# Kernel tuning notes

Measured on AMD Instinct MI355X. Metric: run time of the kernel, lower is better.

Reference implementation:

```python
import jax, jax.numpy as jnp
import numpy as np

# Module scale: T timesteps, N nodes, E directed edges
T, N, E = 6, 20000, 320000
IN_F, HID, OUT_F, K = 11, 64, 3, 2  # K=2 Chebyshev graph conv


def setup_inputs() -> dict:
    key = jax.random.key(0)
    ks = jax.random.split(key, 8)
    X_seq = jax.random.normal(ks[0], (T, N, IN_F), dtype=jnp.float32)
    # col 6 is physical time; make it a monotone ramp so dt != 0 between steps
    X_seq = X_seq.at[:, :, 6].set(jnp.arange(T, dtype=jnp.float32)[:, None] * 0.01)
    edge = jax.random.randint(ks[1], (2, E), 0, N)
    s = 0.05
    # 6 ChebConvs inside GConvGRU, stacked by gate order (z, r, h)
    Wx = jax.random.normal(ks[2], (3, K, IN_F, HID), dtype=jnp.float32) * s
    Wh = jax.random.normal(ks[3], (3, K, HID, HID), dtype=jnp.float32) * s
    bx = jax.random.normal(ks[4], (3, HID), dtype=jnp.float32) * s
    bh = jax.random.normal(ks[5], (3, HID), dtype=jnp.float32) * s
    head_W = jax.random.normal(ks[6], (HID, OUT_F), dtype=jnp.float32) * s
    head_b = jnp.zeros((OUT_F,), dtype=jnp.float32)
    return dict(X_seq=X_seq, edge=edge, Wx=Wx, bx=bx, Wh=Wh, bh=bh,
                head_W=head_W, head_b=head_b)


def _cheb(x, W, b, src, dst, ew, n):
    # PyG ChebConv (sym norm, lambda_max=2): Lhat = -D^-1/2 A D^-1/2
    # K=2: out = T0(x) @ W0 + T1(x) @ W1 + b, T0 = x, T1 = Lhat x
    out = x @ W[0]
    Tx1 = jax.ops.segment_sum(ew[:, None] * x[src], dst, num_segments=n)  # [N, F]
    return out + Tx1 @ W[1] + b


def _forward(X_seq, edge, Wx, bx, Wh, bh, head_W, head_b):
    n = X_seq.shape[1]
    src, dst = edge[0], edge[1]
    deg = jax.ops.segment_sum(jnp.ones((edge.shape[1],), X_seq.dtype), src,
                              num_segments=n)
    dis = jnp.where(deg > 0, jax.lax.rsqrt(jnp.maximum(deg, 1.0)), 0.0)
    ew = -dis[src] * dis[dst]  # scaled Laplacian edge weights

    def cell(x, h):  # GConvGRU cell
        Z = jax.nn.sigmoid(_cheb(x, Wx[0], bx[0], src, dst, ew, n)
                           + _cheb(h, Wh[0], bh[0], src, dst, ew, n))
        R = jax.nn.sigmoid(_cheb(x, Wx[1], bx[1], src, dst, ew, n)
                           + _cheb(h, Wh[1], bh[1], src, dst, ew, n))
        Ht = jnp.tanh(_cheb(x, Wx[2], bx[2], src, dst, ew, n)
                      + _cheb(h * R, Wh[2], bh[2], src, dst, ew, n))
        return Z * h + (1.0 - Z) * Ht

    X_prev = jnp.concatenate([X_seq[:1], X_seq[:-1]], axis=0)

    def step(carry, xs):
        h, u_prev = carry  # u_prev is detached (stop_gradient) like u.detach()
        x_t, x_pm1, t = xs
        dt = x_t[:, 6] - x_pm1[:, 6]
        dt = jnp.where(t == 0, jnp.ones_like(dt), dt)  # guard; t=0 branch discarded
        v = (u_prev - x_pm1[:, 3:6]) / dt[:, None]
        x_mod = x_t.at[:, 3:6].set(u_prev).at[:, 8:11].set(v)
        x_in = jnp.where(t == 0, x_t, x_mod)
        h = cell(x_in, h)
        u = h @ head_W + head_b
        return (h, jax.lax.stop_gradient(u)), u

    h0 = jnp.zeros((n, Wh.shape[-1]), X_seq.dtype)
    u0 = jnp.zeros((n, head_W.shape[-1]), X_seq.dtype)
    ts = jnp.arange(X_seq.shape[0])
    _, outs = jax.lax.scan(step, (h0, u0), (X_seq, X_prev, ts))
    return outs  # [T, N, out_f]


def reference(X_seq, edge, Wx, bx, Wh, bh, head_W, head_b):
    return _forward(X_seq, edge, Wx, bx, Wh, bh, head_W, head_b)
```

## Files before the change

kernel.cpp:

```cpp
#include <hip/hip_runtime.h>
#include <hip/hip_fp16.h>
#include <math.h>

#define TSTEPS 6
#define NN 20000
#define NE 320000
#define INF 11
#define XPAD 16
#define HID 64
#define OUTF 3
#define NPW 4

__device__ __forceinline__ float bcast(float v, int l) {
    return __uint_as_float(__builtin_amdgcn_readlane(__float_as_uint(v), l));
}

__device__ __forceinline__ float tanh_safe(float a) {
    float e2 = __expf(-2.0f * fabsf(a));
    float t = (1.0f - e2) / (1.0f + e2);
    return copysignf(t, a);
}


__global__ void k_deg(const int* __restrict__ src, float* __restrict__ deg, int E) {
    int e = blockIdx.x * blockDim.x + threadIdx.x;
    if (e < E) atomicAdd(&deg[src[e]], 1.0f);
}

__global__ void k_dis(float* deg, int n) {
    int i = blockIdx.x * blockDim.x + threadIdx.x;
    if (i < n) {
        float d = deg[i];
        deg[i] = d > 0.0f ? rsqrtf(fmaxf(d, 1.0f)) : 0.0f;
    }
}

__global__ void k_ew(const int* __restrict__ src, const int* __restrict__ dst,
                     const float* __restrict__ dis, float* __restrict__ ew, int E) {
    int e = blockIdx.x * blockDim.x + threadIdx.x;
    if (e < E) ew[e] = -dis[src[e]] * dis[dst[e]];
}

__global__ void k_indeg(const int* __restrict__ dst, int* __restrict__ indeg, int E) {
    int e = blockIdx.x * blockDim.x + threadIdx.x;
    if (e < E) atomicAdd(&indeg[dst[e]], 1);
}

__global__ __launch_bounds__(1024) void k_scan(const int* __restrict__ in,
                                               int* __restrict__ out, int n) {
    __shared__ int buf[1024];
    __shared__ int carry;
    if (threadIdx.x == 0) carry = 0;
    __syncthreads();
    for (int base = 0; base < n; base += 1024) {
        int i = base + (int)threadIdx.x;
        int v = (i < n) ? in[i] : 0;
        buf[threadIdx.x] = v;
        __syncthreads();
        for (int off = 1; off < 1024; off <<= 1) {
            int t = (threadIdx.x >= (unsigned)off) ? buf[threadIdx.x - off] : 0;
            __syncthreads();
            buf[threadIdx.x] += t;
            __syncthreads();
        }
        if (i < n) out[i] = carry + buf[threadIdx.x] - v;
        __syncthreads();
        if (threadIdx.x == 0) carry += buf[1023];
        __syncthreads();
    }
    if (threadIdx.x == 0) out[n] = carry;
}

__global__ void k_fill(const int* __restrict__ src, const int* __restrict__ dst,
                       const float* __restrict__ ew, int* __restrict__ cursor,
                       int2* __restrict__ pack, int E) {
    int e = blockIdx.x * blockDim.x + threadIdx.x;
    if (e >= E) return;
    int pos = atomicAdd(&cursor[dst[e]], 1);
    int2 v;
    v.x = src[e];
    v.y = __float_as_int(ew[e]);
    pack[pos] = v;
}

__global__ void k_packh4(const float* __restrict__ Wh, float4* __restrict__ out) {
    int idx = blockIdx.x * blockDim.x + threadIdx.x;
    if (idx >= HID * HID) return;
    int j = idx >> 6, f = idx & 63;
    float4 v;
    v.x = Wh[((0 * 2 + 0) * HID + j) * HID + f];
    v.y = Wh[((0 * 2 + 1) * HID + j) * HID + f];
    v.z = Wh[((1 * 2 + 0) * HID + j) * HID + f];
    v.w = Wh[((1 * 2 + 1) * HID + j) * HID + f];
    out[idx] = v;
}
__global__ void k_packh2(const float* __restrict__ Wh, float2* __restrict__ out) {
    int idx = blockIdx.x * blockDim.x + threadIdx.x;
    if (idx >= HID * HID) return;
    int j = idx >> 6, f = idx & 63;
    float2 v;
    v.x = Wh[((2 * 2 + 0) * HID + j) * HID + f];
    v.y = Wh[((2 * 2 + 1) * HID + j) * HID + f];
    out[idx] = v;
}
__global__ void k_packx4(const float* __restrict__ Wx, float4* __restrict__ out) {
    int idx = blockIdx.x * blockDim.x + threadIdx.x;
    if (idx >= INF * HID) return;
    int i = idx >> 6, f = idx & 63;
    float4 v;
    v.x = Wx[((0 * 2 + 0) * INF + i) * HID + f];
    v.y = Wx[((0 * 2 + 1) * INF + i) * HID + f];
    v.z = Wx[((1 * 2 + 0) * INF + i) * HID + f];
    v.w = Wx[((1 * 2 + 1) * INF + i) * HID + f];
    out[idx] = v;
}
__global__ void k_packx2(const float* __restrict__ Wx, float2* __restrict__ out) {
    int idx = blockIdx.x * blockDim.x + threadIdx.x;
    if (idx >= INF * HID) return;
    int i = idx >> 6, f = idx & 63;
    float2 v;
    v.x = Wx[((2 * 2 + 0) * INF + i) * HID + f];
    v.y = Wx[((2 * 2 + 1) * INF + i) * HID + f];
    out[idx] = v;
}


__global__ void k_xin0(const float* __restrict__ Xt, float* __restrict__ xin,
                       __half* __restrict__ xin16, int n) {
    int i = blockIdx.x * blockDim.x + threadIdx.x;
    if (i >= n) return;
    const float* xt = Xt + (size_t)i * INF;
    float* xo = xin + (size_t)i * XPAD;
    __half* xh = xin16 + (size_t)i * XPAD;
#pragma unroll
    for (int k = 0; k < INF; ++k) { float v = xt[k]; xo[k] = v; xh[k] = __float2half(v); }
#pragma unroll
    for (int k = INF; k < XPAD; ++k) { xo[k] = 0.0f; xh[k] = __float2half(0.0f); }
}

__global__ void k_xin(const float* __restrict__ Xt, const float* __restrict__ Xp,
                      const float* __restrict__ uprev, float* __restrict__ xin,
                      __half* __restrict__ xin16, int n) {
    int i = blockIdx.x * blockDim.x + threadIdx.x;
    if (i >= n) return;
    const float* xt = Xt + (size_t)i * INF;
    const float* xp = Xp + (size_t)i * INF;
    const float* up = uprev + (size_t)i * OUTF;
    float* xo = xin + (size_t)i * XPAD;
    __half* xh = xin16 + (size_t)i * XPAD;
    float dt = xt[6] - xp[6];
    float inv = 1.0f / dt;
    float v[XPAD];
    v[0] = xt[0]; v[1] = xt[1]; v[2] = xt[2];
    v[3] = up[0]; v[4] = up[1]; v[5] = up[2];
    v[6] = xt[6]; v[7] = xt[7];
    v[8] = (up[0] - xp[3]) * inv;
    v[9] = (up[1] - xp[4]) * inv;
    v[10] = (up[2] - xp[5]) * inv;
    v[11] = 0.0f; v[12] = 0.0f; v[13] = 0.0f; v[14] = 0.0f; v[15] = 0.0f;
#pragma unroll
    for (int k = 0; k < XPAD; ++k) { xo[k] = v[k]; xh[k] = __float2half(v[k]); }
}

__global__ __launch_bounds__(256) void k_gz(
    const int* __restrict__ rowstart, const int2* __restrict__ pack,
    const float* __restrict__ xin, const __half* __restrict__ xin16,
    const __half* __restrict__ h16,
    const float4* __restrict__ Wx4, const float* __restrict__ bx,
    const float4* __restrict__ Wh4, const float* __restrict__ bh,
    float* __restrict__ t1x, __half* __restrict__ Zb16,
    __half* __restrict__ hr16, int n) {
    int wid = __builtin_amdgcn_readfirstlane(
        (int)((blockIdx.x * blockDim.x + threadIdx.x) >> 6));
    int wbase = wid * NPW;
    int lane = threadIdx.x & 63;
    int f16i = lane & 15;
    if (wbase >= n) return;

    float thg[NPW], axv[NPW], hv[NPW];
#pragma unroll
    for (int nn = 0; nn < NPW; ++nn) {
        int node = wbase + nn;
        int s = rowstart[node], e = rowstart[node + 1];
        float a0 = 0, a1 = 0, a2 = 0, a3 = 0;
        float c0 = 0, c1 = 0, c2 = 0, c3 = 0;
        int p = s;
        for (; p + 3 < e; p += 4) {
            int2 e0 = pack[p], e1 = pack[p + 1], e2 = pack[p + 2], e3 = pack[p + 3];
            float w0 = __int_as_float(e0.y), w1 = __int_as_float(e1.y);
            float w2 = __int_as_float(e2.y), w3 = __int_as_float(e3.y);
            a0 = fmaf(w0, __half2float(h16[(size_t)e0.x * HID + lane]), a0);
            a1 = fmaf(w1, __half2float(h16[(size_t)e1.x * HID + lane]), a1);
            a2 = fmaf(w2, __half2float(h16[(size_t)e2.x * HID + lane]), a2);
            a3 = fmaf(w3, __half2float(h16[(size_t)e3.x * HID + lane]), a3);
            c0 = fmaf(w0, __half2float(xin16[(size_t)e0.x * XPAD + f16i]), c0);
            c1 = fmaf(w1, __half2float(xin16[(size_t)e1.x * XPAD + f16i]), c1);
            c2 = fmaf(w2, __half2float(xin16[(size_t)e2.x * XPAD + f16i]), c2);
            c3 = fmaf(w3, __half2float(xin16[(size_t)e3.x * XPAD + f16i]), c3);
        }
        for (; p < e; ++p) {
            int2 e0 = pack[p];
            float w0 = __int_as_float(e0.y);
            a0 = fmaf(w0, __half2float(h16[(size_t)e0.x * HID + lane]), a0);
            c0 = fmaf(w0, __half2float(xin16[(size_t)e0.x * XPAD + f16i]), c0);
        }
        thg[nn] = (a0 + a1) + (a2 + a3);
        axv[nn] = (c0 + c1) + (c2 + c3);
        hv[nn] = __half2float(h16[(size_t)node * HID + lane]);
    }
#pragma unroll
    for (int nn = 0; nn < NPW; ++nn)
        if (lane < 16) t1x[(size_t)(wbase + nn) * XPAD + lane] = axv[nn];

    float xrow = xin[(size_t)wbase * XPAD + lane];
    float b0z = bx[0 * HID + lane] + bh[0 * HID + lane];
    float b0r = bx[1 * HID + lane] + bh[1 * HID + lane];
    float az[NPW], ar[NPW];
#pragma unroll
    for (int nn = 0; nn < NPW; ++nn) { az[nn] = b0z; ar[nn] = b0r; }
#pragma unroll
    for (int i = 0; i < INF; ++i) {
        float4 w = Wx4[i * HID + lane];
#pragma unroll
        for (int nn = 0; nn < NPW; ++nn) {
            float xv = bcast(xrow, nn * XPAD + i);
            float tv = bcast(axv[nn], i);
            az[nn] = fmaf(xv, w.x, fmaf(tv, w.y, az[nn]));
            ar[nn] = fmaf(xv, w.z, fmaf(tv, w.w, ar[nn]));
        }
    }
#pragma unroll 8
    for (int j = 0; j < HID; ++j) {
        float4 w = Wh4[j * HID + lane];
#pragma unroll
        for (int nn = 0; nn < NPW; ++nn) {
            float hj = bcast(hv[nn], j);
            float tj = bcast(thg[nn], j);
            az[nn] = fmaf(hj, w.x, fmaf(tj, w.y, az[nn]));
            ar[nn] = fmaf(hj, w.z, fmaf(tj, w.w, ar[nn]));
        }
    }
#pragma unroll
    for (int nn = 0; nn < NPW; ++nn) {
        int node = wbase + nn;
        float Z = 1.0f / (1.0f + __expf(-az[nn]));
        float R = 1.0f / (1.0f + __expf(-ar[nn]));
        Zb16[(size_t)node * HID + lane] = __float2half(Z);
        hr16[(size_t)node * HID + lane] = __float2half(hv[nn] * R);
    }
}

__global__ __launch_bounds__(256) void k_gc(
    const int* __restrict__ rowstart, const int2* __restrict__ pack,
    const float* __restrict__ xin, const float* __restrict__ t1x,
    float* __restrict__ h, __half* __restrict__ h16,
    const __half* __restrict__ hr16,
    const float2* __restrict__ Wx2, const float* __restrict__ bx,
    const float2* __restrict__ Wh2, const float* __restrict__ bh,
    const __half* __restrict__ Zb16,
    const float* __restrict__ hw, const float* __restrict__ hb,
    float* __restrict__ out, int n) {
    int wid = __builtin_amdgcn_readfirstlane(
        (int)((blockIdx.x * blockDim.x + threadIdx.x) >> 6));
    int wbase = wid * NPW;
    int lane = threadIdx.x & 63;
    if (wbase >= n) return;

    float thg[NPW], hrv[NPW];
#pragma unroll
    for (int nn = 0; nn < NPW; ++nn) {
        int node = wbase + nn;
        int s = rowstart[node], e = rowstart[node + 1];
        float a0 = 0, a1 = 0, a2 = 0, a3 = 0;
        int p = s;
        for (; p + 3 < e; p += 4) {
            int2 e0 = pack[p], e1 = pack[p + 1], e2 = pack[p + 2], e3 = pack[p + 3];
            a0 = fmaf(__int_as_float(e0.y), __half2float(hr16[(size_t)e0.x * HID + lane]), a0);
            a1 = fmaf(__int_as_float(e1.y), __half2float(hr16[(size_t)e1.x * HID + lane]), a1);
            a2 = fmaf(__int_as_float(e2.y), __half2float(hr16[(size_t)e2.x * HID + lane]), a2);
            a3 = fmaf(__int_as_float(e3.y), __half2float(hr16[(size_t)e3.x * HID + lane]), a3);
        }
        for (; p < e; ++p) {
            int2 e0 = pack[p];
            a0 = fmaf(__int_as_float(e0.y), __half2float(hr16[(size_t)e0.x * HID + lane]), a0);
        }
        thg[nn] = (a0 + a1) + (a2 + a3);
        hrv[nn] = __half2float(hr16[(size_t)node * HID + lane]);
    }

    float xrow = xin[(size_t)wbase * XPAD + lane];
    float trow = t1x[(size_t)wbase * XPAD + lane];
    float b0 = bx[2 * HID + lane] + bh[2 * HID + lane];
    float ah[NPW];
#pragma unroll
    for (int nn = 0; nn < NPW; ++nn) ah[nn] = b0;
#pragma unroll
    for (int i = 0; i < INF; ++i) {
        float2 w = Wx2[i * HID + lane];
#pragma unroll
        for (int nn = 0; nn < NPW; ++nn) {
            float xv = bcast(xrow, nn * XPAD + i);
            float tv = bcast(trow, nn * XPAD + i);
            ah[nn] = fmaf(xv, w.x, fmaf(tv, w.y, ah[nn]));
        }
    }
#pragma unroll 8
    for (int j = 0; j < HID; ++j) {
        float2 w = Wh2[j * HID + lane];
#pragma unroll
        for (int nn = 0; nn < NPW; ++nn) {
            float hj = bcast(hrv[nn], j);
            float tj = bcast(thg[nn], j);
            ah[nn] = fmaf(hj, w.x, fmaf(tj, w.y, ah[nn]));
        }
    }
#pragma unroll
    for (int nn = 0; nn < NPW; ++nn) {
        int node = wbase + nn;
        float Ht = tanh_safe(ah[nn]);
        float z = __half2float(Zb16[(size_t)node * HID + lane]);
        float hv = h[(size_t)node * HID + lane];
        float hnew = z * hv + (1.0f - z) * Ht;
        h[(size_t)node * HID + lane] = hnew;
        h16[(size_t)node * HID + lane] = __float2half(hnew);
#pragma unroll
        for (int o = 0; o < OUTF; ++o) {
            float v = hnew * hw[lane * OUTF + o];
            for (int off = 32; off; off >>= 1) v += __shfl_down(v, off);
            if (lane == 0) out[(size_t)node * OUTF + o] = v + hb[o];
        }
    }
}

extern "C" void kernel_launch(void* const* d_in, const int* in_sizes, int n_in,
                              void* d_out, int out_size, void* d_ws, size_t ws_size,
                              hipStream_t stream) {
    const float* X_seq = (const float*)d_in[0];
    const int* edge = (const int*)d_in[1];
    const float* Wx = (const float*)d_in[2];
    const float* bx = (const float*)d_in[3];
    const float* Wh = (const float*)d_in[4];
    const float* bh = (const float*)d_in[5];
    const float* head_W = (const float*)d_in[6];
    const float* head_b = (const float*)d_in[7];
    float* out = (float*)d_out;

    const int* src = edge;
    const int* dst = edge + NE;

    float* ws = (float*)d_ws;
    float4* Wh4g = (float4*)ws;
    float4* Wx4g = (float4*)(ws + 16384);
    float2* Wh2c = (float2*)(ws + 16384 + 2816);
    float2* Wx2c = (float2*)(ws + 16384 + 2816 + 8192);
    float* fbase = ws + 28800;
    float* dis   = fbase;
    float* ew    = dis + NN;
    float* xin   = ew + NE;
    float* t1x   = xin + NN * XPAD;
    float* h     = t1x + NN * XPAD;
    int* indeg    = (int*)(h + NN * HID);
    int* rowstart = indeg + NN;
    int* cursor   = rowstart + NN + 2;
    int2* pack    = (int2*)(cursor + NN);
    __half* h16   = (__half*)(pack + NE);
    __half* hr16  = h16 + (size_t)NN * HID;
    __half* Zb16  = hr16 + (size_t)NN * HID;
    __half* xin16 = Zb16 + (size_t)NN * HID;

    hipMemsetAsync(dis, 0, NN * sizeof(float), stream);
    hipMemsetAsync(indeg, 0, NN * sizeof(int), stream);
    k_deg<<<(NE + 255) / 256, 256, 0, stream>>>(src, dis, NE);
    k_dis<<<(NN + 255) / 256, 256, 0, stream>>>(dis, NN);
    k_ew<<<(NE + 255) / 256, 256, 0, stream>>>(src, dst, dis, ew, NE);
    k_indeg<<<(NE + 255) / 256, 256, 0, stream>>>(dst, indeg, NE);
    k_scan<<<1, 1024, 0, stream>>>(indeg, rowstart, NN);
    hipMemcpyAsync(cursor, rowstart, NN * sizeof(int), hipMemcpyDeviceToDevice, stream);
    k_fill<<<(NE + 255) / 256, 256, 0, stream>>>(src, dst, ew, cursor, pack, NE);
    k_packh4<<<(HID * HID + 255) / 256, 256, 0, stream>>>(Wh, Wh4g);
    k_packh2<<<(HID * HID + 255) / 256, 256, 0, stream>>>(Wh, Wh2c);
    k_packx4<<<(INF * HID + 255) / 256, 256, 0, stream>>>(Wx, Wx4g);
    k_packx2<<<(INF * HID + 255) / 256, 256, 0, stream>>>(Wx, Wx2c);

    hipMemsetAsync(h, 0, NN * HID * sizeof(float), stream);
    hipMemsetAsync(h16, 0, NN * HID * sizeof(__half), stream);

    const int fused_grid = (NN + 4 * NPW - 1) / (4 * NPW);

    for (int t = 0; t < TSTEPS; ++t) {
        const float* Xt = X_seq + (size_t)t * NN * INF;

        if (t == 0) {
            k_xin0<<<(NN + 255) / 256, 256, 0, stream>>>(Xt, xin, xin16, NN);
        } else {
            const float* Xp = X_seq + (size_t)(t - 1) * NN * INF;
            const float* uprev = out + (size_t)(t - 1) * NN * OUTF;
            k_xin<<<(NN + 255) / 256, 256, 0, stream>>>(Xt, Xp, uprev, xin, xin16, NN);
        }

        k_gz<<<fused_grid, 256, 0, stream>>>(rowstart, pack, xin, xin16, h16,
                                             Wx4g, bx, Wh4g, bh,
                                             t1x, Zb16, hr16, NN);

        k_gc<<<fused_grid, 256, 0, stream>>>(rowstart, pack, xin, t1x, h, h16, hr16,
                                             Wx2c, bx, Wh2c, bh, Zb16,
                                             head_W, head_b,
                                             out + (size_t)t * NN * OUTF, NN);
    }
}
```

Baseline: 531.3 us.

## Pad CSR rows to multiples of 8, fuse input prep into gate kernel, parallelize setup

Each CSR row is padded to a multiple of 8 zero-weight entries, so the gather loops run an 8-wide unrolled body with no scalar tail. In k_gz the x-feature aggregation is split across four 16-lane groups and combined with shuffles. The per-step k_xin kernel is removed: the next step's input row is built inside k_gc from the freshly computed head outputs. Setup is also consolidated: one counting kernel, a three-phase parallel scan replacing the single-block scan, edge weights computed inside fill, one weight-pack kernel, and a zeroing kernel. The padding adds extra zero-weight gathers from node 0, and the pack buffer must be memset each call.

```diff
diff --git a/kernel.cpp b/kernel.cpp
--- a/kernel.cpp
+++ b/kernel.cpp
@@ -10,6 +10,8 @@
 #define HID 64
 #define OUTF 3
 #define NPW 4
+#define EPMAX (NE + 7 * NN)
+#define NB ((NN + 255) / 256)
 
 __device__ __forceinline__ float bcast(float v, int l) {
     return __uint_as_float(__builtin_amdgcn_readlane(__float_as_uint(v), l));
@@ -22,108 +24,124 @@
 }
 
 
-__global__ void k_deg(const int* __restrict__ src, float* __restrict__ deg, int E) {
+__global__ void k_cnt(const int* __restrict__ src, const int* __restrict__ dst,
+                      int* __restrict__ degi, int* __restrict__ indeg, int E) {
     int e = blockIdx.x * blockDim.x + threadIdx.x;
-    if (e < E) atomicAdd(&deg[src[e]], 1.0f);
-}
-
-__global__ void k_dis(float* deg, int n) {
+    if (e >= E) return;
+    atomicAdd(&degi[src[e]], 1);
+    atomicAdd(&indeg[dst[e]], 1);
+}
+
+__global__ void k_dis(const int* __restrict__ degi, float* __restrict__ dis, int n) {
     int i = blockIdx.x * blockDim.x + threadIdx.x;
     if (i < n) {
-        float d = deg[i];
-        deg[i] = d > 0.0f ? rsqrtf(fmaxf(d, 1.0f)) : 0.0f;
-    }
-}
-
-__global__ void k_ew(const int* __restrict__ src, const int* __restrict__ dst,
-                     const float* __restrict__ dis, float* __restrict__ ew, int E) {
-    int e = blockIdx.x * blockDim.x + threadIdx.x;
-    if (e < E) ew[e] = -dis[src[e]] * dis[dst[e]];
-}
-
-__global__ void k_indeg(const int* __restrict__ dst, int* __restrict__ indeg, int E) {
-    int e = blockIdx.x * blockDim.x + threadIdx.x;
-    if (e < E) atomicAdd(&indeg[dst[e]], 1);
-}
-
-__global__ __launch_bounds__(1024) void k_scan(const int* __restrict__ in,
-                                               int* __restrict__ out, int n) {
-    __shared__ int buf[1024];
-    __shared__ int carry;
-    if (threadIdx.x == 0) carry = 0;
+        float d = (float)degi[i];
+        dis[i] = d > 0.0f ? rsqrtf(fmaxf(d, 1.0f)) : 0.0f;
+    }
+}
+
+__global__ __launch_bounds__(256) void k_scanA(const int* __restrict__ indeg,
+                                               int* __restrict__ part,
+                                               int* __restrict__ bsum, int n) {
+    int idx = blockIdx.x * 256 + threadIdx.x;
+    int lane = threadIdx.x & 63, wv = threadIdx.x >> 6;
+    int v = (idx < n) ? ((indeg[idx] + 7) & ~7) : 0;
+#pragma unroll
+    for (int off = 1; off < 64; off <<= 1) {
+        int t = __shfl_up(v, off);
+        if (lane >= off) v += t;
+    }
+    __shared__ int wsum[4];
+    if (lane == 63) wsum[wv] = v;
     __syncthreads();
-    for (int base = 0; base < n; base += 1024) {
-        int i = base + (int)threadIdx.x;
-        int v = (i < n) ? in[i] : 0;
-        buf[threadIdx.x] = v;
-        __syncthreads();
-        for (int off = 1; off < 1024; off <<= 1) {
-            int t = (threadIdx.x >= (unsigned)off) ? buf[threadIdx.x - off] : 0;
-            __syncthreads();
-            buf[threadIdx.x] += t;
-            __syncthreads();
-        }
-        if (i < n) out[i] = carry + buf[threadIdx.x] - v;
-        __syncthreads();
-        if (threadIdx.x == 0) carry += buf[1023];
-        __syncthreads();
-    }
-    if (threadIdx.x == 0) out[n] = carry;
+    int add = 0;
+    for (int w = 0; w < wv; ++w) add += wsum[w];
+    v += add;
+    if (idx < n) part[idx] = v;
+    if (threadIdx.x == 255) bsum[blockIdx.x] = v;
+}
+
+__global__ __launch_bounds__(128) void k_scanB(const int* __restrict__ bsum,
+                                               int* __restrict__ boff, int nb) {
+    int tid = threadIdx.x;
+    int lane = tid & 63, wv = tid >> 6;
+    int orig = (tid < nb) ? bsum[tid] : 0;
+    int v = orig;
+#pragma unroll
+    for (int off = 1; off < 64; off <<= 1) {
+        int t = __shfl_up(v, off);
+        if (lane >= off) v += t;
+    }
+    __shared__ int w0;
+    if (lane == 63 && wv == 0) w0 = v;
+    __syncthreads();
+    if (wv == 1) v += w0;
+    if (tid < nb) boff[tid] = v - orig;
+}
+
+__global__ __launch_bounds__(256) void k_scanC(const int* __restrict__ indeg,
+                                               int* __restrict__ part,
+                                               const int* __restrict__ boff,
+                                               int* __restrict__ cursor, int n) {
+    int idx = blockIdx.x * 256 + threadIdx.x;
+    if (idx >= n) return;
+    int pd = (indeg[idx] + 7) & ~7;
+    int incl = part[idx] + boff[blockIdx.x];
+    int excl = incl - pd;
+    part[idx] = excl;
+    cursor[idx] = excl;
+    if (idx == n - 1) part[n] = incl;
 }
 
 __global__ void k_fill(const int* __restrict__ src, const int* __restrict__ dst,
-                       const float* __restrict__ ew, int* __restrict__ cursor,
+                       const float* __restrict__ dis, int* __restrict__ cursor,
                        int2* __restrict__ pack, int E) {
     int e = blockIdx.x * blockDim.x + threadIdx.x;
     if (e >= E) return;
-    int pos = atomicAdd(&cursor[dst[e]], 1);
+    int s = src[e], d = dst[e];
+    int pos = atomicAdd(&cursor[d], 1);
     int2 v;
-    v.x = src[e];
-    v.y = __float_as_int(ew[e]);
+    v.x = s;
+    v.y = __float_as_int(-dis[s] * dis[d]);
     pack[pos] = v;
 }
 
-__global__ void k_packh4(const float* __restrict__ Wh, float4* __restrict__ out) {
+__global__ void k_pack(const float* __restrict__ Wh, const float* __restrict__ Wx,
+                       float4* __restrict__ Wh4, float2* __restrict__ Wh2,
+                       float4* __restrict__ Wx4, float2* __restrict__ Wx2) {
     int idx = blockIdx.x * blockDim.x + threadIdx.x;
-    if (idx >= HID * HID) return;
-    int j = idx >> 6, f = idx & 63;
-    float4 v;
-    v.x = Wh[((0 * 2 + 0) * HID + j) * HID + f];
-    v.y = Wh[((0 * 2 + 1) * HID + j) * HID + f];
-    v.z = Wh[((1 * 2 + 0) * HID + j) * HID + f];
-    v.w = Wh[((1 * 2 + 1) * HID + j) * HID + f];
-    out[idx] = v;
-}
-__global__ void k_packh2(const float* __restrict__ Wh, float2* __restrict__ out) {
-    int idx = blockIdx.x * blockDim.x + threadIdx.x;
-    if (idx >= HID * HID) return;
-    int j = idx >> 6, f = idx & 63;
-    float2 v;
-    v.x = Wh[((2 * 2 + 0) * HID + j) * HID + f];
-    v.y = Wh[((2 * 2 + 1) * HID + j) * HID + f];
-    out[idx] = v;
-}
-__global__ void k_packx4(const float* __restrict__ Wx, float4* __restrict__ out) {
-    int idx = blockIdx.x * blockDim.x + threadIdx.x;
-    if (idx >= INF * HID) return;
-    int i = idx >> 6, f = idx & 63;
-    float4 v;
-    v.x = Wx[((0 * 2 + 0) * INF + i) * HID + f];
-    v.y = Wx[((0 * 2 + 1) * INF + i) * HID + f];
-    v.z = Wx[((1 * 2 + 0) * INF + i) * HID + f];
-    v.w = Wx[((1 * 2 + 1) * INF + i) * HID + f];
-    out[idx] = v;
-}
-__global__ void k_packx2(const float* __restrict__ Wx, float2* __restrict__ out) {
-    int idx = blockIdx.x * blockDim.x + threadIdx.x;
-    if (idx >= INF * HID) return;
-    int i = idx >> 6, f = idx & 63;
-    float2 v;
-    v.x = Wx[((2 * 2 + 0) * INF + i) * HID + f];
-    v.y = Wx[((2 * 2 + 1) * INF + i) * HID + f];
-    out[idx] = v;
-}
-
+    if (idx < HID * HID) {
+        int j = idx >> 6, f = idx & 63;
+        float4 v4;
+        v4.x = Wh[((0 * 2 + 0) * HID + j) * HID + f];
+        v4.y = Wh[((0 * 2 + 1) * HID + j) * HID + f];
+        v4.z = Wh[((1 * 2 + 0) * HID + j) * HID + f];
+        v4.w = Wh[((1 * 2 + 1) * HID + j) * HID + f];
+        Wh4[idx] = v4;
+        float2 v2;
+        v2.x = Wh[((2 * 2 + 0) * HID + j) * HID + f];
+        v2.y = Wh[((2 * 2 + 1) * HID + j) * HID + f];
+        Wh2[idx] = v2;
+    } else if (idx < HID * HID + INF * HID) {
+        int k = idx - HID * HID;
+        int i = k >> 6, f = k & 63;
+        float4 v4;
+        v4.x = Wx[((0 * 2 + 0) * INF + i) * HID + f];
+        v4.y = Wx[((0 * 2 + 1) * INF + i) * HID + f];
+        v4.z = Wx[((1 * 2 + 0) * INF + i) * HID + f];
+        v4.w = Wx[((1 * 2 + 1) * INF + i) * HID + f];
+        Wx4[k] = v4;
+        float2 v2;
+        v2.x = Wx[((2 * 2 + 0) * INF + i) * HID + f];
+        v2.y = Wx[((2 * 2 + 1) * INF + i) * HID + f];
+        Wx2[k] = v2;
+    }
+}
+
+__global__ void k_hzero(float* __restrict__ h, __half* __restrict__ h16, int nel) {
+    int i = blockIdx.x * blockDim.x + threadIdx.x;
+    if (i < nel) { h[i] = 0.0f; h16[i] = __float2half(0.0f); }
+}
 
 __global__ void k_xin0(const float* __restrict__ Xt, float* __restrict__ xin,
                        __half* __restrict__ xin16, int n) {
@@ -138,29 +156,6 @@
     for (int k = INF; k < XPAD; ++k) { xo[k] = 0.0f; xh[k] = __float2half(0.0f); }
 }
 
-__global__ void k_xin(const float* __restrict__ Xt, const float* __restrict__ Xp,
-                      const float* __restrict__ uprev, float* __restrict__ xin,
-                      __half* __restrict__ xin16, int n) {
-    int i = blockIdx.x * blockDim.x + threadIdx.x;
-    if (i >= n) return;
-    const float* xt = Xt + (size_t)i * INF;
-    const float* xp = Xp + (size_t)i * INF;
-    const float* up = uprev + (size_t)i * OUTF;
-    float* xo = xin + (size_t)i * XPAD;
-    __half* xh = xin16 + (size_t)i * XPAD;
-    float dt = xt[6] - xp[6];
-    float inv = 1.0f / dt;
-    float v[XPAD];
-    v[0] = xt[0]; v[1] = xt[1]; v[2] = xt[2];
-    v[3] = up[0]; v[4] = up[1]; v[5] = up[2];
-    v[6] = xt[6]; v[7] = xt[7];
-    v[8] = (up[0] - xp[3]) * inv;
-    v[9] = (up[1] - xp[4]) * inv;
-    v[10] = (up[2] - xp[5]) * inv;
-    v[11] = 0.0f; v[12] = 0.0f; v[13] = 0.0f; v[14] = 0.0f; v[15] = 0.0f;
-#pragma unroll
-    for (int k = 0; k < XPAD; ++k) { xo[k] = v[k]; xh[k] = __float2half(v[k]); }
-}
 
 __global__ __launch_bounds__(256) void k_gz(
     const int* __restrict__ rowstart, const int2* __restrict__ pack,
@@ -174,7 +169,7 @@
         (int)((blockIdx.x * blockDim.x + threadIdx.x) >> 6));
     int wbase = wid * NPW;
     int lane = threadIdx.x & 63;
-    int f16i = lane & 15;
+    int f16i = lane & 15, eo = lane >> 4;
     if (wbase >= n) return;
 
     float thg[NPW], axv[NPW], hv[NPW];
@@ -183,29 +178,34 @@
         int node = wbase + nn;
         int s = rowstart[node], e = rowstart[node + 1];
         float a0 = 0, a1 = 0, a2 = 0, a3 = 0;
-        float c0 = 0, c1 = 0, c2 = 0, c3 = 0;
-        int p = s;
-        for (; p + 3 < e; p += 4) {
-            int2 e0 = pack[p], e1 = pack[p + 1], e2 = pack[p + 2], e3 = pack[p + 3];
+        float c0 = 0, c1 = 0;
+        for (int p = s; p < e; p += 8) {
+            int2 e0 = pack[p],     e1 = pack[p + 1], e2 = pack[p + 2], e3 = pack[p + 3];
+            int2 e4 = pack[p + 4], e5 = pack[p + 5], e6 = pack[p + 6], e7 = pack[p + 7];
             float w0 = __int_as_float(e0.y), w1 = __int_as_float(e1.y);
             float w2 = __int_as_float(e2.y), w3 = __int_as_float(e3.y);
+            float w4 = __int_as_float(e4.y), w5 = __int_as_float(e5.y);
+            float w6 = __int_as_float(e6.y), w7 = __int_as_float(e7.y);
             a0 = fmaf(w0, __half2float(h16[(size_t)e0.x * HID + lane]), a0);
             a1 = fmaf(w1, __half2float(h16[(size_t)e1.x * HID + lane]), a1);
             a2 = fmaf(w2, __half2float(h16[(size_t)e2.x * HID + lane]), a2);
             a3 = fmaf(w3, __half2float(h16[(size_t)e3.x * HID + lane]), a3);
-            c0 = fmaf(w0, __half2float(xin16[(size_t)e0.x * XPAD + f16i]), c0);
-            c1 = fmaf(w1, __half2float(xin16[(size_t)e1.x * XPAD + f16i]), c1);
-            c2 = fmaf(w2, __half2float(xin16[(size_t)e2.x * XPAD + f16i]), c2);
-            c3 = fmaf(w3, __half2float(xin16[(size_t)e3.x * XPAD + f16i]), c3);
-        }
-        for (; p < e; ++p) {
-            int2 e0 = pack[p];
-            float w0 = __int_as_float(e0.y);
-            a0 = fmaf(w0, __half2float(h16[(size_t)e0.x * HID + lane]), a0);
-            c0 = fmaf(w0, __half2float(xin16[(size_t)e0.x * XPAD + f16i]), c0);
+            a0 = fmaf(w4, __half2float(h16[(size_t)e4.x * HID + lane]), a0);
+            a1 = fmaf(w5, __half2float(h16[(size_t)e5.x * HID + lane]), a1);
+            a2 = fmaf(w6, __half2float(h16[(size_t)e6.x * HID + lane]), a2);
+            a3 = fmaf(w7, __half2float(h16[(size_t)e7.x * HID + lane]), a3);
+            int sx0 = (eo == 0) ? e0.x : (eo == 1) ? e2.x : (eo == 2) ? e4.x : e6.x;
+            float wx0 = (eo == 0) ? w0 : (eo == 1) ? w2 : (eo == 2) ? w4 : w6;
+            int sx1 = (eo == 0) ? e1.x : (eo == 1) ? e3.x : (eo == 2) ? e5.x : e7.x;
+            float wx1 = (eo == 0) ? w1 : (eo == 1) ? w3 : (eo == 2) ? w5 : w7;
+            c0 = fmaf(wx0, __half2float(xin16[(size_t)sx0 * XPAD + f16i]), c0);
+            c1 = fmaf(wx1, __half2float(xin16[(size_t)sx1 * XPAD + f16i]), c1);
         }
         thg[nn] = (a0 + a1) + (a2 + a3);
-        axv[nn] = (c0 + c1) + (c2 + c3);
+        float cx = c0 + c1;
+        cx += __shfl_down(cx, 32);
+        cx += __shfl_down(cx, 16);
+        axv[nn] = cx;
         hv[nn] = __half2float(h16[(size_t)node * HID + lane]);
     }
 #pragma unroll
@@ -259,7 +259,10 @@
     const float2* __restrict__ Wh2, const float* __restrict__ bh,
     const __half* __restrict__ Zb16,
     const float* __restrict__ hw, const float* __restrict__ hb,
-    float* __restrict__ out, int n) {
+    float* __restrict__ out,
+    const float* __restrict__ Xcur, const float* __restrict__ Xnxt,
+    float* __restrict__ xin_w, __half* __restrict__ xin16_w,
+    int last, int n) {
     int wid = __builtin_amdgcn_readfirstlane(
         (int)((blockIdx.x * blockDim.x + threadIdx.x) >> 6));
     int wbase = wid * NPW;
@@ -272,17 +275,17 @@
         int node = wbase + nn;
         int s = rowstart[node], e = rowstart[node + 1];
         float a0 = 0, a1 = 0, a2 = 0, a3 = 0;
-        int p = s;
-        for (; p + 3 < e; p += 4) {
-            int2 e0 = pack[p], e1 = pack[p + 1], e2 = pack[p + 2], e3 = pack[p + 3];
+        for (int p = s; p < e; p += 8) {
+            int2 e0 = pack[p],     e1 = pack[p + 1], e2 = pack[p + 2], e3 = pack[p + 3];
+            int2 e4 = pack[p + 4], e5 = pack[p + 5], e6 = pack[p + 6], e7 = pack[p + 7];
             a0 = fmaf(__int_as_float(e0.y), __half2float(hr16[(size_t)e0.x * HID + lane]), a0);
             a1 = fmaf(__int_as_float(e1.y), __half2float(hr16[(size_t)e1.x * HID + lane]), a1);
             a2 = fmaf(__int_as_float(e2.y), __half2float(hr16[(size_t)e2.x * HID + lane]), a2);
             a3 = fmaf(__int_as_float(e3.y), __half2float(hr16[(size_t)e3.x * HID + lane]), a3);
-        }
-        for (; p < e; ++p) {
-            int2 e0 = pack[p];
-            a0 = fmaf(__int_as_float(e0.y), __half2float(hr16[(size_t)e0.x * HID + lane]), a0);
+            a0 = fmaf(__int_as_float(e4.y), __half2float(hr16[(size_t)e4.x * HID + lane]), a0);
+            a1 = fmaf(__int_as_float(e5.y), __half2float(hr16[(size_t)e5.x * HID + lane]), a1);
+            a2 = fmaf(__int_as_float(e6.y), __half2float(hr16[(size_t)e6.x * HID + lane]), a2);
+            a3 = fmaf(__int_as_float(e7.y), __half2float(hr16[(size_t)e7.x * HID + lane]), a3);
         }
         thg[nn] = (a0 + a1) + (a2 + a3);
         hrv[nn] = __half2float(hr16[(size_t)node * HID + lane]);
@@ -319,15 +322,49 @@
         int node = wbase + nn;
         float Ht = tanh_safe(ah[nn]);
         float z = __half2float(Zb16[(size_t)node * HID + lane]);
-        float hv = h[(size_t)node * HID + lane];
-        float hnew = z * hv + (1.0f - z) * Ht;
+        float hvv = h[(size_t)node * HID + lane];
+        float hnew = z * hvv + (1.0f - z) * Ht;
         h[(size_t)node * HID + lane] = hnew;
         h16[(size_t)node * HID + lane] = __float2half(hnew);
-#pragma unroll
-        for (int o = 0; o < OUTF; ++o) {
-            float v = hnew * hw[lane * OUTF + o];
-            for (int off = 32; off; off >>= 1) v += __shfl_down(v, off);
-            if (lane == 0) out[(size_t)node * OUTF + o] = v + hb[o];
+        float u0, u1, u2;
+        {
+            float v0 = hnew * hw[lane * OUTF + 0];
+            float v1 = hnew * hw[lane * OUTF + 1];
+            float v2 = hnew * hw[lane * OUTF + 2];
+            for (int off = 32; off; off >>= 1) {
+                v0 += __shfl_down(v0, off);
+                v1 += __shfl_down(v1, off);
+                v2 += __shfl_down(v2, off);
+            }
+            u0 = bcast(v0, 0) + hb[0];
+            u1 = bcast(v1, 0) + hb[1];
+            u2 = bcast(v2, 0) + hb[2];
+        }
+        if (lane == 0) {
+            float* o = out + (size_t)node * OUTF;
+            o[0] = u0; o[1] = u1; o[2] = u2;
+        }
+        if (!last) {
+            const float* x1r = Xnxt + (size_t)node * INF;
+            const float* x0r = Xcur + (size_t)node * INF;
+            float x1 = (lane < INF) ? x1r[lane] : 0.0f;
+            float x0v = (lane >= 3 && lane < 7) ? x0r[lane] : 0.0f;
+            float dt = bcast(x1, 6) - bcast(x0v, 6);
+            float inv = 1.0f / dt;
+            float c3 = bcast(x0v, 3), c4 = bcast(x0v, 4), c5 = bcast(x0v, 5);
+            float val;
+            if (lane < 3) val = x1;
+            else if (lane < 6) val = (lane == 3) ? u0 : (lane == 4) ? u1 : u2;
+            else if (lane < 8) val = x1;
+            else if (lane < 11) {
+                float uu = (lane == 8) ? u0 : (lane == 9) ? u1 : u2;
+                float cc = (lane == 8) ? c3 : (lane == 9) ? c4 : c5;
+                val = (uu - cc) * inv;
+            } else val = 0.0f;
+            if (lane < XPAD) {
+                xin_w[(size_t)node * XPAD + lane] = val;
+                xin16_w[(size_t)node * XPAD + lane] = __float2half(val);
+            }
         }
     }
 }
@@ -351,60 +388,53 @@
     float* ws = (float*)d_ws;
     float4* Wh4g = (float4*)ws;
     float4* Wx4g = (float4*)(ws + 16384);
-    float2* Wh2c = (float2*)(ws + 16384 + 2816);
-    float2* Wx2c = (float2*)(ws + 16384 + 2816 + 8192);
+    float2* Wh2c = (float2*)(ws + 19200);
+    float2* Wx2c = (float2*)(ws + 27392);
     float* fbase = ws + 28800;
-    float* dis   = fbase;
-    float* ew    = dis + NN;
-    float* xin   = ew + NE;
-    float* t1x   = xin + NN * XPAD;
-    float* h     = t1x + NN * XPAD;
-    int* indeg    = (int*)(h + NN * HID);
+    float* dis  = fbase;
+    float* xin  = dis + NN;
+    float* t1x  = xin + (size_t)NN * XPAD;
+    float* h    = t1x + (size_t)NN * XPAD;
+    int* degi     = (int*)(h + (size_t)NN * HID);
+    int* indeg    = degi + NN;
     int* rowstart = indeg + NN;
     int* cursor   = rowstart + NN + 2;
-    int2* pack    = (int2*)(cursor + NN);
-    __half* h16   = (__half*)(pack + NE);
+    int* bsum     = cursor + NN;
+    int* boff     = bsum + 128;
+    int2* pack    = (int2*)(boff + 128);
+    __half* h16   = (__half*)(pack + EPMAX);
     __half* hr16  = h16 + (size_t)NN * HID;
     __half* Zb16  = hr16 + (size_t)NN * HID;
     __half* xin16 = Zb16 + (size_t)NN * HID;
 
-    hipMemsetAsync(dis, 0, NN * sizeof(float), stream);
-    hipMemsetAsync(indeg, 0, NN * sizeof(int), stream);
-    k_deg<<<(NE + 255) / 256, 256, 0, stream>>>(src, dis, NE);
-    k_dis<<<(NN + 255) / 256, 256, 0, stream>>>(dis, NN);
-    k_ew<<<(NE + 255) / 256, 256, 0, stream>>>(src, dst, dis, ew, NE);
-    k_indeg<<<(NE + 255) / 256, 256, 0, stream>>>(dst, indeg, NE);
-    k_scan<<<1, 1024, 0, stream>>>(indeg, rowstart, NN);
-    hipMemcpyAsync(cursor, rowstart, NN * sizeof(int), hipMemcpyDeviceToDevice, stream);
-    k_fill<<<(NE + 255) / 256, 256, 0, stream>>>(src, dst, ew, cursor, pack, NE);
-    k_packh4<<<(HID * HID + 255) / 256, 256, 0, stream>>>(Wh, Wh4g);
-    k_packh2<<<(HID * HID + 255) / 256, 256, 0, stream>>>(Wh, Wh2c);
-    k_packx4<<<(INF * HID + 255) / 256, 256, 0, stream>>>(Wx, Wx4g);
-    k_packx2<<<(INF * HID + 255) / 256, 256, 0, stream>>>(Wx, Wx2c);
-
-    hipMemsetAsync(h, 0, NN * HID * sizeof(float), stream);
-    hipMemsetAsync(h16, 0, NN * HID * sizeof(__half), stream);
+    hipMemsetAsync(degi, 0, 2 * NN * sizeof(int), stream);
+    hipMemsetAsync(pack, 0, (size_t)EPMAX * sizeof(int2), stream);
+    k_cnt<<<(NE + 255) / 256, 256, 0, stream>>>(src, dst, degi, indeg, NE);
+    k_dis<<<(NN + 255) / 256, 256, 0, stream>>>(degi, dis, NN);
+    k_scanA<<<NB, 256, 0, stream>>>(indeg, rowstart, bsum, NN);
+    k_scanB<<<1, 128, 0, stream>>>(bsum, boff, NB);
+    k_scanC<<<NB, 256, 0, stream>>>(indeg, rowstart, boff, cursor, NN);
+    k_fill<<<(NE + 255) / 256, 256, 0, stream>>>(src, dst, dis, cursor, pack, NE);
+    k_pack<<<(HID * HID + INF * HID + 255) / 256, 256, 0, stream>>>(
+        Wh, Wx, Wh4g, Wh2c, Wx4g, Wx2c);
+    k_hzero<<<(NN * HID + 255) / 256, 256, 0, stream>>>(h, h16, NN * HID);
+
+    k_xin0<<<(NN + 255) / 256, 256, 0, stream>>>(X_seq, xin, xin16, NN);
 
     const int fused_grid = (NN + 4 * NPW - 1) / (4 * NPW);
 
     for (int t = 0; t < TSTEPS; ++t) {
-        const float* Xt = X_seq + (size_t)t * NN * INF;
-
-        if (t == 0) {
-            k_xin0<<<(NN + 255) / 256, 256, 0, stream>>>(Xt, xin, xin16, NN);
-        } else {
-            const float* Xp = X_seq + (size_t)(t - 1) * NN * INF;
-            const float* uprev = out + (size_t)(t - 1) * NN * OUTF;
-            k_xin<<<(NN + 255) / 256, 256, 0, stream>>>(Xt, Xp, uprev, xin, xin16, NN);
-        }
-
         k_gz<<<fused_grid, 256, 0, stream>>>(rowstart, pack, xin, xin16, h16,
                                              Wx4g, bx, Wh4g, bh,
                                              t1x, Zb16, hr16, NN);
 
+        const float* Xcur = X_seq + (size_t)t * NN * INF;
+        const float* Xnxt = (t + 1 < TSTEPS) ? X_seq + (size_t)(t + 1) * NN * INF : X_seq;
         k_gc<<<fused_grid, 256, 0, stream>>>(rowstart, pack, xin, t1x, h, h16, hr16,
                                              Wx2c, bx, Wh2c, bh, Zb16,
                                              head_W, head_b,
-                                             out + (size_t)t * NN * OUTF, NN);
-    }
-}
+                                             out + (size_t)t * NN * OUTF,
+                                             Xcur, Xnxt, xin, xin16,
+                                             (t + 1 == TSTEPS) ? 1 : 0, NN);
+    }
+}
```

After: 442.9 us. 16.6% less time.
